# Optimization experiments

Measured on AMD Instinct MI355X. Metric: run time of the kernel, lower is better.

## Reference

```python
import jax, jax.numpy as jnp
import numpy as np
import math

EMBED_DIM = 1024
MEMORY_DIM = 1024
MEMORY_SIZE = 2048
B, S = 8, 4096


def bitnet_linear(x, W, b):
    """Eval-mode BitNetLinear: 1.58-bit weight quant + 8-bit activation quant."""
    w_scale = jnp.mean(jnp.abs(W))
    qW = jnp.sign(W) * (jnp.abs(W) > 0.5 * w_scale).astype(W.dtype)
    i_scale = jnp.max(jnp.abs(x)) / 127.0
    qx = jnp.clip(jnp.round(x / i_scale), -128.0, 127.0)
    out = jnp.einsum('bsi,oi->bso', qx, qW) * (w_scale * i_scale)
    return out + b


def setup_inputs() -> dict:
    key = jax.random.key(0)
    ks = jax.random.split(key, 9)
    return {
        'x': jax.random.normal(ks[0], (B, S, EMBED_DIM), jnp.float32),
        'memory_keys': jax.random.normal(ks[1], (MEMORY_SIZE, MEMORY_DIM), jnp.float32),
        'memory_values': jax.random.normal(ks[2], (MEMORY_SIZE, EMBED_DIM), jnp.float32),
        'Wk': jax.random.normal(ks[3], (MEMORY_DIM, EMBED_DIM), jnp.float32) * 0.1,
        'bk': jnp.zeros((MEMORY_DIM,), jnp.float32),
        'Wv': jax.random.normal(ks[4], (EMBED_DIM, EMBED_DIM), jnp.float32) * 0.1,
        'bv': jnp.zeros((EMBED_DIM,), jnp.float32),
        'Wo': jax.random.normal(ks[5], (EMBED_DIM, EMBED_DIM), jnp.float32) * 0.1,
        'bo': jnp.zeros((EMBED_DIM,), jnp.float32),
    }


def reference(x, memory_keys, memory_values, Wk, bk, Wv, bv, Wo, bo):
    # quantized key/value projections
    query_keys = bitnet_linear(x, Wk, bk)          # [B, S, Dm]
    _query_values = bitnet_linear(x, Wv, bv)       # computed in original (used only by update path)
    # memory cross-attention over fixed bank
    similarities = jnp.einsum('bsd,md->bsm', query_keys, memory_keys)  # [B, S, M]
    attention_weights = jax.nn.softmax(similarities / math.sqrt(MEMORY_DIM), axis=-1)
    retrieved = jnp.einsum('bsm,me->bse', attention_weights, memory_values)  # [B, S, E]
    output = bitnet_linear(x + retrieved, Wo, bo)
    return output
```

## Files before the change

### kernel.cpp

```cpp
#include <hip/hip_runtime.h>
#include <hip/hip_bf16.h>
#include <stdint.h>
#include <type_traits>

typedef __attribute__((ext_vector_type(8))) short bf16x8;
typedef __attribute__((ext_vector_type(4))) float f32x4;
typedef __attribute__((ext_vector_type(4))) int i32x4;

struct Scalars {
  double sum_wk;
  double sum_wo;
  unsigned int max_x_bits;
  unsigned int max_y_bits;
};

__device__ __forceinline__ unsigned short f2bf(float f) {
  __hip_bfloat16 h = __float2bfloat16(f);
  return *reinterpret_cast<unsigned short*>(&h);
}

__device__ __forceinline__ void async16(void* lds, const void* g) {
  __builtin_amdgcn_global_load_lds((__attribute__((address_space(1))) void*)g,
                                   (__attribute__((address_space(3))) void*)lds, 16, 0, 0);
}

__device__ __forceinline__ void tile_swizzle(int nxShift, int& bx, int& by) {
  const int per = gridDim.x >> 3;
  const int tile = (blockIdx.x & 7) * per + (blockIdx.x >> 3);
  bx = tile & ((1 << nxShift) - 1);
  by = tile >> nxShift;
}

__device__ __forceinline__ f32x4 mm(bf16x8 a, bf16x8 b, f32x4 c) {
  return __builtin_amdgcn_mfma_f32_16x16x32_bf16(a, b, c, 0, 0, 0);
}
__device__ __forceinline__ i32x4 mm(i32x4 a, i32x4 b, i32x4 c) {
  return __builtin_amdgcn_mfma_i32_16x16x64_i8(a, b, c, 0, 0, 0);
}

__global__ __launch_bounds__(256) void abssum_kernel(const float* __restrict__ w, size_t n,
                                                     double* __restrict__ out) {
  size_t tid = (size_t)blockIdx.x * blockDim.x + threadIdx.x;
  size_t stride = (size_t)gridDim.x * blockDim.x;
  double s = 0.0;
  for (size_t i = tid * 4; i < n; i += stride * 4) {
    float4 v = *(const float4*)(w + i);
    s += (double)fabsf(v.x) + (double)fabsf(v.y) + (double)fabsf(v.z) + (double)fabsf(v.w);
  }
#pragma unroll
  for (int o = 32; o > 0; o >>= 1) s += __shfl_xor(s, o);
  __shared__ double sm[4];
  if ((threadIdx.x & 63) == 0) sm[threadIdx.x >> 6] = s;
  __syncthreads();
  if (threadIdx.x == 0) atomicAdd(out, sm[0] + sm[1] + sm[2] + sm[3]);
}

__global__ __launch_bounds__(256) void absmax_kernel(const float* __restrict__ x, size_t n,
                                                     unsigned int* __restrict__ out) {
  size_t tid = (size_t)blockIdx.x * blockDim.x + threadIdx.x;
  size_t stride = (size_t)gridDim.x * blockDim.x;
  float m = 0.0f;
  for (size_t i = tid * 4; i < n; i += stride * 4) {
    float4 v = *(const float4*)(x + i);
    m = fmaxf(m, fmaxf(fmaxf(fabsf(v.x), fabsf(v.y)), fmaxf(fabsf(v.z), fabsf(v.w))));
  }
#pragma unroll
  for (int o = 32; o > 0; o >>= 1) m = fmaxf(m, __shfl_xor(m, o));
  __shared__ float sm[4];
  if ((threadIdx.x & 63) == 0) sm[threadIdx.x >> 6] = m;
  __syncthreads();
  if (threadIdx.x == 0)
    atomicMax(out, __float_as_uint(fmaxf(fmaxf(sm[0], sm[1]), fmaxf(sm[2], sm[3]))));
}

__global__ __launch_bounds__(256) void quant_act_i8_kernel(const float* __restrict__ x,
                                                           char* __restrict__ q,
                                                           const unsigned int* __restrict__ maxbits,
                                                           size_t n) {
  const float isc = __uint_as_float(*maxbits) / 127.0f;
  size_t tid = (size_t)blockIdx.x * blockDim.x + threadIdx.x;
  size_t stride = (size_t)gridDim.x * blockDim.x;
  for (size_t i = tid * 4; i < n; i += stride * 4) {
    float4 v = *(const float4*)(x + i);
    char4 o;
    o.x = (char)(int)fminf(fmaxf(rintf(v.x / isc), -128.f), 127.f);
    o.y = (char)(int)fminf(fmaxf(rintf(v.y / isc), -128.f), 127.f);
    o.z = (char)(int)fminf(fmaxf(rintf(v.z / isc), -128.f), 127.f);
    o.w = (char)(int)fminf(fmaxf(rintf(v.w / isc), -128.f), 127.f);
    *(char4*)(q + i) = o;
  }
}

__global__ __launch_bounds__(256) void quant_w_i8_kernel(const float* __restrict__ W,
                                                         char* __restrict__ qW,
                                                         const double* __restrict__ sum, size_t n) {
  const float wsc = (float)(*sum / (double)n);
  const float thr = 0.5f * wsc;
  size_t tid = (size_t)blockIdx.x * blockDim.x + threadIdx.x;
  size_t stride = (size_t)gridDim.x * blockDim.x;
  for (size_t i = tid * 4; i < n; i += stride * 4) {
    float4 v = *(const float4*)(W + i);
    char4 o;
    o.x = (char)(fabsf(v.x) > thr ? (v.x > 0.f ? 1 : -1) : 0);
    o.y = (char)(fabsf(v.y) > thr ? (v.y > 0.f ? 1 : -1) : 0);
    o.z = (char)(fabsf(v.z) > thr ? (v.z > 0.f ? 1 : -1) : 0);
    o.w = (char)(fabsf(v.w) > thr ? (v.w > 0.f ? 1 : -1) : 0);
    *(char4*)(qW + i) = o;
  }
}

__global__ __launch_bounds__(256) void cast_bf16_kernel(const float* __restrict__ src,
                                                        __hip_bfloat16* __restrict__ dst,
                                                        size_t n) {
  size_t tid = (size_t)blockIdx.x * blockDim.x + threadIdx.x;
  size_t stride = (size_t)gridDim.x * blockDim.x;
  for (size_t i = tid * 4; i < n; i += stride * 4) {
    float4 v = *(const float4*)(src + i);
    ushort4 o;
    o.x = f2bf(v.x); o.y = f2bf(v.y); o.z = f2bf(v.z); o.w = f2bf(v.w);
    *(ushort4*)((unsigned short*)dst + i) = o;
  }
}

__global__ void transpose_mv_kernel(const float* __restrict__ mv,
                                    __hip_bfloat16* __restrict__ mvT) {
  __shared__ float tile[32][33];
  int tx = threadIdx.x, ty = threadIdx.y;
  int e = blockIdx.x * 32 + tx;
  int m = blockIdx.y * 32 + ty;
  tile[ty][tx] = mv[(size_t)m * 1024 + e];
  __syncthreads();
  int om = blockIdx.y * 32 + tx;
  mvT[(size_t)(blockIdx.x * 32 + ty) * 2048 + om] = __float2bfloat16(tile[tx][ty]);
}

__global__ __launch_bounds__(256) void softmax_kernel(__hip_bfloat16* __restrict__ sims) {
  unsigned short* row = (unsigned short*)(sims + (size_t)blockIdx.x * 2048);
  const int t = threadIdx.x;
  const int l = t & 63, wv = t >> 6;
  uint4 r4 = *(const uint4*)(row + t * 8);
  float v[8];
  v[0] = __uint_as_float(r4.x << 16); v[1] = __uint_as_float(r4.x & 0xffff0000u);
  v[2] = __uint_as_float(r4.y << 16); v[3] = __uint_as_float(r4.y & 0xffff0000u);
  v[4] = __uint_as_float(r4.z << 16); v[5] = __uint_as_float(r4.z & 0xffff0000u);
  v[6] = __uint_as_float(r4.w << 16); v[7] = __uint_as_float(r4.w & 0xffff0000u);
  float m = v[0];
#pragma unroll
  for (int i = 1; i < 8; ++i) m = fmaxf(m, v[i]);
#pragma unroll
  for (int o = 32; o > 0; o >>= 1) m = fmaxf(m, __shfl_xor(m, o));
  __shared__ float red[4], red2[4];
  if (l == 0) red[wv] = m;
  __syncthreads();
  m = fmaxf(fmaxf(red[0], red[1]), fmaxf(red[2], red[3]));
  float s = 0.f;
#pragma unroll
  for (int i = 0; i < 8; ++i) { v[i] = expf(v[i] - m); s += v[i]; }
#pragma unroll
  for (int o = 32; o > 0; o >>= 1) s += __shfl_xor(s, o);
  if (l == 0) red2[wv] = s;
  __syncthreads();
  s = red2[0] + red2[1] + red2[2] + red2[3];
  unsigned short b[8];
#pragma unroll
  for (int i = 0; i < 8; ++i) b[i] = f2bf(v[i] / s);
  uint4 o4;
  o4.x = (unsigned)b[0] | ((unsigned)b[1] << 16);
  o4.y = (unsigned)b[2] | ((unsigned)b[3] << 16);
  o4.z = (unsigned)b[4] | ((unsigned)b[5] << 16);
  o4.w = (unsigned)b[6] | ((unsigned)b[7] << 16);
  *(uint4*)(row + t * 8) = o4;
}

#define CFENCE() asm volatile("" ::: "memory")
#define BAR8() { CFENCE(); __builtin_amdgcn_s_barrier(); CFENCE(); }
#define WLGKM(N) { asm volatile("s_waitcnt lgkmcnt(" #N ")" ::: "memory"); __builtin_amdgcn_sched_barrier(0); }
#define WVM(N) asm volatile("s_waitcnt vmcnt(" #N ")" ::: "memory")

template <int EPI>
__global__ __launch_bounds__(512, 2) void gemm8(
    const char* __restrict__ A, const char* __restrict__ B, void* __restrict__ C,
    const float* __restrict__ aux, Scalars* __restrict__ sc,
    int Ndim, int KB, int nxShift) {
  constexpr bool I8 = (EPI >= 3);
  using FR  = typename std::conditional<I8, i32x4, bf16x8>::type;
  using ACC = typename std::conditional<I8, i32x4, f32x4>::type;
  __shared__ __align__(16) char lds[4][2][16384];

  int bx, by;
  tile_swizzle(nxShift, bx, by);
  const int rowBlk = by * 256, colBlk = bx * 256;

  const int t = threadIdx.x, w = t >> 6, l = t & 63;
  const int wm = w >> 2, wn = w & 3;
  const int quad = l >> 4, m16 = l & 15;
  const int NT = KB >> 7, NIT = NT >> 1;

  int voA[2][2], voB[2][2];
#pragma unroll
  for (int hf = 0; hf < 2; ++hf)
#pragma unroll
    for (int j = 0; j < 2; ++j) {
      const int idx = j * 64 + (t >> 3);
      const int kby = ((t & 7) ^ (idx & 7)) << 4;
      voA[hf][j] = (rowBlk + ((idx >> 6) << 7) + (hf << 6) + (idx & 63)) * KB + kby;
      voB[hf][j] = (colBlk + ((idx >> 5) << 6) + (hf << 5) + (idx & 31)) * KB + kby;
    }

  const char* baA[2];
  const char* baB[2];
#pragma unroll
  for (int ks = 0; ks < 2; ++ks) {
    const int x16 = ((ks << 6) + (quad << 4)) ^ ((m16 & 7) << 4);
    baA[ks] = &lds[0][0][(wm * 64 + m16) * 128 + x16];
    baB[ks] = &lds[2][0][(wn * 32 + m16) * 128 + x16];
  }

#define STG_A(slot, hf, tk)                                                         \
  if ((tk) < NT) {                                                                  \
    _Pragma("unroll") for (int j = 0; j < 2; ++j)                                   \
      async16(&lds[hf][slot][j * 8192 + (w << 10)],                                 \
              A + (((size_t)(tk)) << 7) + voA[hf][j]);                              \
  }
#define STG_B(slot, hf, tk)                                                         \
  if ((tk) < NT) {                                                                  \
    _Pragma("unroll") for (int j = 0; j < 2; ++j)                                   \
      async16(&lds[2 + (hf)][slot][j * 8192 + (w << 10)],                           \
              B + (((size_t)(tk)) << 7) + voB[hf][j]);                              \
  }

#define LD_A(dst, slot, hf, f, ks) \
  dst = *(const FR*)(baA[ks] + ((hf)*32768 + (slot)*16384 + (f)*2048));
#define LD_B(dst, slot, hf, gg, ks) \
  dst = *(const FR*)(baB[ks] + ((hf)*32768 + (slot)*16384 + (gg)*2048));

#define R_A0(s) { _Pragma("unroll") for (int f_ = 0; f_ < 4; ++f_) { LD_A(af[f_][0], s, 0, f_, 0); LD_A(af[f_][1], s, 0, f_, 1); } }
#define R_A1(s) { _Pragma("unroll") for (int f_ = 0; f_ < 4; ++f_) { LD_A(af[f_][0], s, 1, f_, 0); LD_A(af[f_][1], s, 1, f_, 1); } }
#define R_B0(s) { _Pragma("unroll") for (int g_ = 0; g_ < 2; ++g_) { LD_B(b0[g_][0], s, 0, g_, 0); LD_B(b0[g_][1], s, 0, g_, 1); } }
#define R_B1(s) { _Pragma("unroll") for (int g_ = 0; g_ < 2; ++g_) { LD_B(b1[g_][0], s, 1, g_, 0); LD_B(b1[g_][1], s, 1, g_, 1); } }

#define MM8(FO, GO, BR)                                                             \
  __builtin_amdgcn_s_setprio(1);                                                    \
  _Pragma("unroll") for (int f_ = 0; f_ < 4; ++f_)                                  \
    _Pragma("unroll") for (int g_ = 0; g_ < 2; ++g_) {                              \
      acc[(FO) + f_][(GO) + g_] = mm(af[f_][0], BR[g_][0], acc[(FO) + f_][(GO) + g_]); \
      acc[(FO) + f_][(GO) + g_] = mm(af[f_][1], BR[g_][1], acc[(FO) + f_][(GO) + g_]); \
    }                                                                               \
  __builtin_amdgcn_s_setprio(0);

#define TSTEP(s, tk, last)                                                          \
  {                                                                                 \
                     \
    R_B1(s);                                                                        \
    STG_A((s) ^ 1, 1, (tk) + 1);                                                    \
    BAR8(); WLGKM(4);                                                               \
    MM8(0, 0, b0);                                                                  \
    BAR8();                                                                         \
        \
    STG_A(s, 0, (tk) + 2);                                                          \
    BAR8(); WLGKM(0);                                                               \
    MM8(0, 2, b1);                                                                  \
    R_A1(s);                                                                        \
    BAR8();                                                                         \
                                                                \
    STG_B(s, 0, (tk) + 2);                                                          \
    BAR8(); WLGKM(0);                                                               \
    MM8(4, 0, b0);                                                                  \
    BAR8();                                                                         \
           \
    STG_B(s, 1, (tk) + 2);                                                          \
    if (last) { WVM(0); } else { WVM(6); }                                          \
    BAR8();                                                                         \
    MM8(4, 2, b1);                                                                  \
    R_A0((s) ^ 1);                                                                  \
    R_B0((s) ^ 1);                                                                  \
    BAR8();                                                                         \
  }

  FR af[4][2], b0[2][2], b1[2][2];
  ACC acc[8][4] = {};

  STG_A(0, 0, 0); STG_B(0, 0, 0); STG_B(0, 1, 0); STG_A(0, 1, 0);
  CFENCE();
  STG_A(1, 0, 1); STG_B(1, 0, 1); STG_B(1, 1, 1);
  WVM(6);
  BAR8();
  R_A0(0); R_B0(0);

  for (int it = 0; it < NIT; ++it) {
    const bool last = (it == NIT - 1);
    TSTEP(0, it * 2, last);
    TSTEP(1, it * 2 + 1, last);
  }

  float sK = 0.0f;
  if constexpr (EPI == 3)
    sK = (float)(sc->sum_wk * (1.0 / 1048576.0)) * (__uint_as_float(sc->max_x_bits) / 127.0f);
  if constexpr (EPI == 4)
    sK = (float)(sc->sum_wo * (1.0 / 1048576.0)) * (__uint_as_float(sc->max_y_bits) / 127.0f);

  float amax = 0.0f;
#pragma unroll
  for (int f = 0; f < 8; ++f) {
#pragma unroll
    for (int g = 0; g < 4; ++g) {
      const int col = colBlk + wn * 64 + g * 16 + m16;
#pragma unroll
      for (int rg = 0; rg < 4; ++rg) {
        const int row = rowBlk + wm * 128 + f * 16 + quad * 4 + rg;
        if constexpr (EPI == 1) {
          ((__hip_bfloat16*)C)[(size_t)row * Ndim + col] =
              __float2bfloat16(acc[f][g][rg] * 0.03125f);
        } else if constexpr (EPI == 2) {
          float v = acc[f][g][rg] + aux[(size_t)row * Ndim + col];
          ((float*)C)[(size_t)row * Ndim + col] = v;
          amax = fmaxf(amax, fabsf(v));
        } else if constexpr (EPI == 3) {
          ((__hip_bfloat16*)C)[(size_t)row * Ndim + col] =
              __float2bfloat16((float)acc[f][g][rg] * sK + aux[col]);
        } else {
          ((float*)C)[(size_t)row * Ndim + col] = (float)acc[f][g][rg] * sK + aux[col];
        }
      }
    }
  }

  if constexpr (EPI == 2) {
    __shared__ float wred[8];
#pragma unroll
    for (int o = 32; o > 0; o >>= 1) amax = fmaxf(amax, __shfl_xor(amax, o));
    if (l == 0) wred[w] = amax;
    __syncthreads();
    if (t == 0) {
      float m = wred[0];
#pragma unroll
      for (int i = 1; i < 8; ++i) m = fmaxf(m, wred[i]);
      atomicMax(&sc->max_y_bits, __float_as_uint(m));
    }
  }
#undef STG_A
#undef STG_B
#undef LD_A
#undef LD_B
#undef R_A0
#undef R_A1
#undef R_B0
#undef R_B1
#undef MM8
#undef TSTEP
}

extern "C" void kernel_launch(void* const* d_in, const int* in_sizes, int n_in,
                              void* d_out, int out_size, void* d_ws, size_t ws_size,
                              hipStream_t stream) {
  (void)in_sizes; (void)n_in; (void)out_size; (void)ws_size;
  const float* x  = (const float*)d_in[0];
  const float* mk = (const float*)d_in[1];
  const float* mv = (const float*)d_in[2];
  const float* Wk = (const float*)d_in[3];
  const float* bk = (const float*)d_in[4];
  const float* Wo = (const float*)d_in[7];
  const float* bo = (const float*)d_in[8];
  float* out = (float*)d_out;

  const int M = 32768, E = 1024, MEM = 2048;

  char* ws = (char*)d_ws;
  Scalars* sc = (Scalars*)ws;
  const size_t off0 = 256;
  char* qx8 = ws + off0;
  __hip_bfloat16* qk = (__hip_bfloat16*)(ws + off0 + (size_t)M * E);
  float* y = (float*)(ws + off0);
  const size_t off1 = off0 + (size_t)M * E * 4;
  __hip_bfloat16* sims = (__hip_bfloat16*)(ws + off1);
  char* qy8 = (char*)sims;
  const size_t off2 = off1 + (size_t)M * MEM * 2;
  char* qWk8 = ws + off2;
  char* qWo8 = qWk8 + (size_t)E * E;
  __hip_bfloat16* mkb = (__hip_bfloat16*)(qWo8 + (size_t)E * E);
  __hip_bfloat16* mvT = mkb + (size_t)MEM * E;

  hipMemsetAsync(ws, 0, 256, stream);

  abssum_kernel<<<dim3(256), dim3(256), 0, stream>>>(Wk, (size_t)E * E, &sc->sum_wk);
  abssum_kernel<<<dim3(256), dim3(256), 0, stream>>>(Wo, (size_t)E * E, &sc->sum_wo);
  absmax_kernel<<<dim3(2048), dim3(256), 0, stream>>>(x, (size_t)M * E, &sc->max_x_bits);

  quant_act_i8_kernel<<<dim3(2048), dim3(256), 0, stream>>>(x, qx8, &sc->max_x_bits, (size_t)M * E);
  quant_w_i8_kernel<<<dim3(256), dim3(256), 0, stream>>>(Wk, qWk8, &sc->sum_wk, (size_t)E * E);
  quant_w_i8_kernel<<<dim3(256), dim3(256), 0, stream>>>(Wo, qWo8, &sc->sum_wo, (size_t)E * E);
  cast_bf16_kernel<<<dim3(256), dim3(256), 0, stream>>>(mk, mkb, (size_t)MEM * E);
  transpose_mv_kernel<<<dim3(E / 32, MEM / 32), dim3(32, 32), 0, stream>>>(mv, mvT);

  gemm8<3><<<dim3((E / 256) * (M / 256)), dim3(512), 0, stream>>>(
      qx8, qWk8, qk, bk, sc, E, E, 2);
  gemm8<1><<<dim3((MEM / 256) * (M / 256)), dim3(512), 0, stream>>>(
      (const char*)qk, (const char*)mkb, sims, nullptr, sc, MEM, 2 * E, 3);
  softmax_kernel<<<dim3(M), dim3(256), 0, stream>>>(sims);
  gemm8<2><<<dim3((E / 256) * (M / 256)), dim3(512), 0, stream>>>(
      (const char*)sims, (const char*)mvT, y, x, sc, E, 2 * MEM, 2);
  quant_act_i8_kernel<<<dim3(2048), dim3(256), 0, stream>>>(y, qy8, &sc->max_y_bits, (size_t)M * E);
  gemm8<4><<<dim3((E / 256) * (M / 256)), dim3(512), 0, stream>>>(
      qy8, qWo8, out, bo, sc, E, E, 2);
}
```

Before: 774.4 us.

## Make GEMMs persistent over multiple column tiles with continuous K pipeline

The GEMM kernel becomes persistent: each of 256 blocks processes several 256-wide column tiles for one row block, and the async global-to-LDS prefetch runs across tile boundaries so the pipeline never drains between tiles. The per-step barrier/lgkm waits are restructured and B-fragment reads are moved to the end of the step. The weight abssum and quantization kernels are each merged into one two-way launch. This is meant to cut wave-launch tails, pipeline fill/drain and launch overhead, at the cost of less parallelism per launch (256 blocks) and more complex synchronization that could introduce LDS hazards.

```diff
diff --git a/kernel.cpp b/kernel.cpp
--- a/kernel.cpp
+++ b/kernel.cpp
@@ -24,13 +24,6 @@
                                    (__attribute__((address_space(3))) void*)lds, 16, 0, 0);
 }
 
-__device__ __forceinline__ void tile_swizzle(int nxShift, int& bx, int& by) {
-  const int per = gridDim.x >> 3;
-  const int tile = (blockIdx.x & 7) * per + (blockIdx.x >> 3);
-  bx = tile & ((1 << nxShift) - 1);
-  by = tile >> nxShift;
-}
-
 __device__ __forceinline__ f32x4 mm(bf16x8 a, bf16x8 b, f32x4 c) {
   return __builtin_amdgcn_mfma_f32_16x16x32_bf16(a, b, c, 0, 0, 0);
 }
@@ -38,8 +31,11 @@
   return __builtin_amdgcn_mfma_i32_16x16x64_i8(a, b, c, 0, 0, 0);
 }
 
-__global__ __launch_bounds__(256) void abssum_kernel(const float* __restrict__ w, size_t n,
-                                                     double* __restrict__ out) {
+__global__ __launch_bounds__(256) void abssum2_kernel(const float* __restrict__ wa,
+                                                      const float* __restrict__ wb,
+                                                      double* __restrict__ out) {
+  const float* w = blockIdx.y ? wb : wa;
+  const size_t n = 1048576;
   size_t tid = (size_t)blockIdx.x * blockDim.x + threadIdx.x;
   size_t stride = (size_t)gridDim.x * blockDim.x;
   double s = 0.0;
@@ -52,7 +48,7 @@
   __shared__ double sm[4];
   if ((threadIdx.x & 63) == 0) sm[threadIdx.x >> 6] = s;
   __syncthreads();
-  if (threadIdx.x == 0) atomicAdd(out, sm[0] + sm[1] + sm[2] + sm[3]);
+  if (threadIdx.x == 0) atomicAdd(&out[blockIdx.y], sm[0] + sm[1] + sm[2] + sm[3]);
 }
 
 __global__ __launch_bounds__(256) void absmax_kernel(const float* __restrict__ x, size_t n,
@@ -91,10 +87,15 @@
   }
 }
 
-__global__ __launch_bounds__(256) void quant_w_i8_kernel(const float* __restrict__ W,
-                                                         char* __restrict__ qW,
-                                                         const double* __restrict__ sum, size_t n) {
-  const float wsc = (float)(*sum / (double)n);
+__global__ __launch_bounds__(256) void quant_w2_kernel(const float* __restrict__ Wk,
+                                                       const float* __restrict__ Wo,
+                                                       char* __restrict__ qk8,
+                                                       char* __restrict__ qo8,
+                                                       const double* __restrict__ sums) {
+  const float* W = blockIdx.y ? Wo : Wk;
+  char* q = blockIdx.y ? qo8 : qk8;
+  const size_t n = 1048576;
+  const float wsc = (float)(sums[blockIdx.y] * (1.0 / 1048576.0));
   const float thr = 0.5f * wsc;
   size_t tid = (size_t)blockIdx.x * blockDim.x + threadIdx.x;
   size_t stride = (size_t)gridDim.x * blockDim.x;
@@ -105,7 +106,7 @@
     o.y = (char)(fabsf(v.y) > thr ? (v.y > 0.f ? 1 : -1) : 0);
     o.z = (char)(fabsf(v.z) > thr ? (v.z > 0.f ? 1 : -1) : 0);
     o.w = (char)(fabsf(v.w) > thr ? (v.w > 0.f ? 1 : -1) : 0);
-    *(char4*)(qW + i) = o;
+    *(char4*)(q + i) = o;
   }
 }
 
@@ -172,29 +173,31 @@
   *(uint4*)(row + t * 8) = o4;
 }
 
-#define CFENCE() asm volatile("" ::: "memory")
-#define BAR8() { CFENCE(); __builtin_amdgcn_s_barrier(); CFENCE(); }
-#define WLGKM(N) { asm volatile("s_waitcnt lgkmcnt(" #N ")" ::: "memory"); __builtin_amdgcn_sched_barrier(0); }
+#define BAR8() { __builtin_amdgcn_sched_barrier(0); asm volatile("" ::: "memory"); \
+                 __builtin_amdgcn_s_barrier(); asm volatile("" ::: "memory"); }
 #define WVM(N) asm volatile("s_waitcnt vmcnt(" #N ")" ::: "memory")
 
-template <int EPI>
-__global__ __launch_bounds__(512, 2) void gemm8(
+template <int EPI, int NTS, int TPB>
+__global__ __launch_bounds__(512, 2) void gemm8p(
     const char* __restrict__ A, const char* __restrict__ B, void* __restrict__ C,
-    const float* __restrict__ aux, Scalars* __restrict__ sc,
-    int Ndim, int KB, int nxShift) {
+    const float* __restrict__ aux, Scalars* __restrict__ sc, int Ndim) {
   constexpr bool I8 = (EPI >= 3);
   using FR  = typename std::conditional<I8, i32x4, bf16x8>::type;
   using ACC = typename std::conditional<I8, i32x4, f32x4>::type;
+  constexpr int NT = 1 << NTS;
+  constexpr int KTOT = NT * TPB;
+  constexpr int KB = 128 << NTS;
   __shared__ __align__(16) char lds[4][2][16384];
 
-  int bx, by;
-  tile_swizzle(nxShift, bx, by);
-  const int rowBlk = by * 256, colBlk = bx * 256;
+  const int lin = ((blockIdx.x & 7) << 5) + (blockIdx.x >> 3);
+  const int by = lin >> 1;
+  const int bx0 = (lin & 1) * TPB;
+  const int rowBlk = by * 256;
+  const int colBlk0 = bx0 * 256;
 
   const int t = threadIdx.x, w = t >> 6, l = t & 63;
   const int wm = w >> 2, wn = w & 3;
   const int quad = l >> 4, m16 = l & 15;
-  const int NT = KB >> 7, NIT = NT >> 1;
 
   int voA[2][2], voB[2][2];
 #pragma unroll
@@ -204,7 +207,7 @@
       const int idx = j * 64 + (t >> 3);
       const int kby = ((t & 7) ^ (idx & 7)) << 4;
       voA[hf][j] = (rowBlk + ((idx >> 6) << 7) + (hf << 6) + (idx & 63)) * KB + kby;
-      voB[hf][j] = (colBlk + ((idx >> 5) << 6) + (hf << 5) + (idx & 31)) * KB + kby;
+      voB[hf][j] = (((idx >> 5) << 6) + (hf << 5) + (idx & 31)) * KB + kby;
     }
 
   const char* baA[2];
@@ -216,17 +219,18 @@
     baB[ks] = &lds[2][0][(wn * 32 + m16) * 128 + x16];
   }
 
-#define STG_A(slot, hf, tk)                                                         \
-  if ((tk) < NT) {                                                                  \
+#define STG_A(slot, hf, kt)                                                         \
+  if ((kt) < KTOT) {                                                                \
+    const char* gp = A + (((kt) & (NT - 1)) << 7);                                  \
     _Pragma("unroll") for (int j = 0; j < 2; ++j)                                   \
-      async16(&lds[hf][slot][j * 8192 + (w << 10)],                                 \
-              A + (((size_t)(tk)) << 7) + voA[hf][j]);                              \
-  }
-#define STG_B(slot, hf, tk)                                                         \
-  if ((tk) < NT) {                                                                  \
+      async16(&lds[hf][slot][j * 8192 + (w << 10)], gp + voA[hf][j]);               \
+  }
+#define STG_B(slot, hf, kt)                                                         \
+  if ((kt) < KTOT) {                                                                \
+    const char* gp = B + (size_t)(colBlk0 + (((kt) >> NTS) << 8)) * KB +            \
+                     (((kt) & (NT - 1)) << 7);                                      \
     _Pragma("unroll") for (int j = 0; j < 2; ++j)                                   \
-      async16(&lds[2 + (hf)][slot][j * 8192 + (w << 10)],                           \
-              B + (((size_t)(tk)) << 7) + voB[hf][j]);                              \
+      async16(&lds[2 + (hf)][slot][j * 8192 + (w << 10)], gp + voB[hf][j]);         \
   }
 
 #define LD_A(dst, slot, hf, f, ks) \
@@ -248,50 +252,31 @@
     }                                                                               \
   __builtin_amdgcn_s_setprio(0);
 
-#define TSTEP(s, tk, last)                                                          \
+#define TSTEP(s, kt, last)                                                          \
   {                                                                                 \
-                     \
-    R_B1(s);                                                                        \
-    STG_A((s) ^ 1, 1, (tk) + 1);                                                    \
-    BAR8(); WLGKM(4);                                                               \
+                                                                  \
+    STG_A((s) ^ 1, 1, (kt) + 1);                                                    \
     MM8(0, 0, b0);                                                                  \
     BAR8();                                                                         \
-        \
-    STG_A(s, 0, (tk) + 2);                                                          \
-    BAR8(); WLGKM(0);                                                               \
+                    \
+    STG_A(s, 0, (kt) + 2);                                                          \
     MM8(0, 2, b1);                                                                  \
     R_A1(s);                                                                        \
     BAR8();                                                                         \
-                                                                \
-    STG_B(s, 0, (tk) + 2);                                                          \
-    BAR8(); WLGKM(0);                                                               \
+                                                                  \
+    STG_B(s, 0, (kt) + 2);                                                          \
     MM8(4, 0, b0);                                                                  \
     BAR8();                                                                         \
-           \
-    STG_B(s, 1, (tk) + 2);                                                          \
+                  \
+    STG_B(s, 1, (kt) + 2);                                                          \
     if (last) { WVM(0); } else { WVM(6); }                                          \
     BAR8();                                                                         \
     MM8(4, 2, b1);                                                                  \
-    R_A0((s) ^ 1);                                                                  \
-    R_B0((s) ^ 1);                                                                  \
-    BAR8();                                                                         \
+    R_A0((s) ^ 1); R_B0((s) ^ 1); R_B1((s) ^ 1);                                    \
   }
 
   FR af[4][2], b0[2][2], b1[2][2];
   ACC acc[8][4] = {};
-
-  STG_A(0, 0, 0); STG_B(0, 0, 0); STG_B(0, 1, 0); STG_A(0, 1, 0);
-  CFENCE();
-  STG_A(1, 0, 1); STG_B(1, 0, 1); STG_B(1, 1, 1);
-  WVM(6);
-  BAR8();
-  R_A0(0); R_B0(0);
-
-  for (int it = 0; it < NIT; ++it) {
-    const bool last = (it == NIT - 1);
-    TSTEP(0, it * 2, last);
-    TSTEP(1, it * 2 + 1, last);
-  }
 
   float sK = 0.0f;
   if constexpr (EPI == 3)
@@ -299,44 +284,54 @@
   if constexpr (EPI == 4)
     sK = (float)(sc->sum_wo * (1.0 / 1048576.0)) * (__uint_as_float(sc->max_y_bits) / 127.0f);
 
-  float amax = 0.0f;
-#pragma unroll
-  for (int f = 0; f < 8; ++f) {
-#pragma unroll
-    for (int g = 0; g < 4; ++g) {
-      const int col = colBlk + wn * 64 + g * 16 + m16;
-#pragma unroll
-      for (int rg = 0; rg < 4; ++rg) {
-        const int row = rowBlk + wm * 128 + f * 16 + quad * 4 + rg;
-        if constexpr (EPI == 1) {
-          ((__hip_bfloat16*)C)[(size_t)row * Ndim + col] =
-              __float2bfloat16(acc[f][g][rg] * 0.03125f);
-        } else if constexpr (EPI == 2) {
-          float v = acc[f][g][rg] + aux[(size_t)row * Ndim + col];
-          ((float*)C)[(size_t)row * Ndim + col] = v;
-          amax = fmaxf(amax, fabsf(v));
-        } else if constexpr (EPI == 3) {
-          ((__hip_bfloat16*)C)[(size_t)row * Ndim + col] =
-              __float2bfloat16((float)acc[f][g][rg] * sK + aux[col]);
-        } else {
-          ((float*)C)[(size_t)row * Ndim + col] = (float)acc[f][g][rg] * sK + aux[col];
+  STG_A(0, 0, 0); STG_B(0, 0, 0); STG_B(0, 1, 0); STG_A(0, 1, 0);
+  STG_A(1, 0, 1); STG_B(1, 0, 1); STG_B(1, 1, 1);
+  WVM(6);
+  BAR8();
+  R_A0(0); R_B0(0); R_B1(0);
+
+  for (int tile = 0; tile < TPB; ++tile) {
+    for (int it = 0; it < NT / 2; ++it) {
+      const int kt = tile * NT + it * 2;
+      TSTEP(0, kt, (kt) >= KTOT - 2);
+      TSTEP(1, kt + 1, (kt + 1) >= KTOT - 2);
+    }
+
+    const int colBlk = (bx0 + tile) * 256;
+    float amax = 0.0f;
+#pragma unroll
+    for (int f = 0; f < 8; ++f) {
+#pragma unroll
+      for (int g = 0; g < 4; ++g) {
+        const int col = colBlk + wn * 64 + g * 16 + m16;
+#pragma unroll
+        for (int rg = 0; rg < 4; ++rg) {
+          const int row = rowBlk + wm * 128 + f * 16 + quad * 4 + rg;
+          if constexpr (EPI == 1) {
+            ((__hip_bfloat16*)C)[(size_t)row * Ndim + col] =
+                __float2bfloat16(acc[f][g][rg] * 0.03125f);
+          } else if constexpr (EPI == 2) {
+            float v = acc[f][g][rg] + aux[(size_t)row * Ndim + col];
+            ((float*)C)[(size_t)row * Ndim + col] = v;
+            amax = fmaxf(amax, fabsf(v));
+          } else if constexpr (EPI == 3) {
+            ((__hip_bfloat16*)C)[(size_t)row * Ndim + col] =
+                __float2bfloat16((float)acc[f][g][rg] * sK + aux[col]);
+          } else {
+            ((float*)C)[(size_t)row * Ndim + col] = (float)acc[f][g][rg] * sK + aux[col];
+          }
         }
       }
     }
-  }
-
-  if constexpr (EPI == 2) {
-    __shared__ float wred[8];
-#pragma unroll
-    for (int o = 32; o > 0; o >>= 1) amax = fmaxf(amax, __shfl_xor(amax, o));
-    if (l == 0) wred[w] = amax;
-    __syncthreads();
-    if (t == 0) {
-      float m = wred[0];
-#pragma unroll
-      for (int i = 1; i < 8; ++i) m = fmaxf(m, wred[i]);
-      atomicMax(&sc->max_y_bits, __float_as_uint(m));
+    if constexpr (EPI == 2) {
+#pragma unroll
+      for (int o = 32; o > 0; o >>= 1) amax = fmaxf(amax, __shfl_xor(amax, o));
+      if (l == 0) atomicMax(&sc->max_y_bits, __float_as_uint(amax));
     }
+#pragma unroll
+    for (int f = 0; f < 8; ++f)
+#pragma unroll
+      for (int g = 0; g < 4; ++g) acc[f][g] = ACC{0, 0, 0, 0};
   }
 #undef STG_A
 #undef STG_B
@@ -382,24 +377,20 @@
 
   hipMemsetAsync(ws, 0, 256, stream);
 
-  abssum_kernel<<<dim3(256), dim3(256), 0, stream>>>(Wk, (size_t)E * E, &sc->sum_wk);
-  abssum_kernel<<<dim3(256), dim3(256), 0, stream>>>(Wo, (size_t)E * E, &sc->sum_wo);
+  abssum2_kernel<<<dim3(256, 2), dim3(256), 0, stream>>>(Wk, Wo, &sc->sum_wk);
   absmax_kernel<<<dim3(2048), dim3(256), 0, stream>>>(x, (size_t)M * E, &sc->max_x_bits);
 
   quant_act_i8_kernel<<<dim3(2048), dim3(256), 0, stream>>>(x, qx8, &sc->max_x_bits, (size_t)M * E);
-  quant_w_i8_kernel<<<dim3(256), dim3(256), 0, stream>>>(Wk, qWk8, &sc->sum_wk, (size_t)E * E);
-  quant_w_i8_kernel<<<dim3(256), dim3(256), 0, stream>>>(Wo, qWo8, &sc->sum_wo, (size_t)E * E);
+  quant_w2_kernel<<<dim3(256, 2), dim3(256), 0, stream>>>(Wk, Wo, qWk8, qWo8, &sc->sum_wk);
   cast_bf16_kernel<<<dim3(256), dim3(256), 0, stream>>>(mk, mkb, (size_t)MEM * E);
   transpose_mv_kernel<<<dim3(E / 32, MEM / 32), dim3(32, 32), 0, stream>>>(mv, mvT);
 
-  gemm8<3><<<dim3((E / 256) * (M / 256)), dim3(512), 0, stream>>>(
-      qx8, qWk8, qk, bk, sc, E, E, 2);
-  gemm8<1><<<dim3((MEM / 256) * (M / 256)), dim3(512), 0, stream>>>(
-      (const char*)qk, (const char*)mkb, sims, nullptr, sc, MEM, 2 * E, 3);
+  gemm8p<3, 3, 2><<<dim3(256), dim3(512), 0, stream>>>(qx8, qWk8, qk, bk, sc, E);
+  gemm8p<1, 4, 4><<<dim3(256), dim3(512), 0, stream>>>(
+      (const char*)qk, (const char*)mkb, sims, nullptr, sc, MEM);
   softmax_kernel<<<dim3(M), dim3(256), 0, stream>>>(sims);
-  gemm8<2><<<dim3((E / 256) * (M / 256)), dim3(512), 0, stream>>>(
-      (const char*)sims, (const char*)mvT, y, x, sc, E, 2 * MEM, 2);
+  gemm8p<2, 5, 2><<<dim3(256), dim3(512), 0, stream>>>(
+      (const char*)sims, (const char*)mvT, y, x, sc, E);
   quant_act_i8_kernel<<<dim3(2048), dim3(256), 0, stream>>>(y, qy8, &sc->max_y_bits, (size_t)M * E);
-  gemm8<4><<<dim3((E / 256) * (M / 256)), dim3(512), 0, stream>>>(
-      qy8, qWo8, out, bo, sc, E, E, 2);
-}
+  gemm8p<4, 3, 2><<<dim3(256), dim3(512), 0, stream>>>(qy8, qWo8, out, bo, sc, E);
+}
```

Measured after the change: 1.025 ms. +32.4%, slower.
